# Kernel optimization log

Measured on AMD Instinct MI355X. Metric: run time of the kernel, lower is better.

The kernel has to match this reference:

```python
import jax, jax.numpy as jnp
import numpy as np

B, L, V, D, C, R = 8, 2048, 32000, 512, 64, 64
NBLK = 2           # n_layers - 1
H = 2 * D          # stem hidden dim
STD = 0.02


def _ln(x, w, b):
    m = x.mean(-1, keepdims=True)
    v = ((x - m) ** 2).mean(-1, keepdims=True)
    return (x - m) / jnp.sqrt(v + 1e-5) * w + b


def setup_inputs() -> dict:
    key = jax.random.key(0)
    ks = jax.random.split(key, 16)
    n = lambda k, shp: jax.random.normal(k, shp, dtype=jnp.float32) * STD
    return {
        "token_ids": jax.random.randint(ks[0], (B, L), 0, V),
        "tok_emb": n(ks[1], (V, D)),
        "pos_emb": n(ks[2], (L, D)),
        "stem_ln_w": jnp.ones((NBLK, D), jnp.float32),
        "stem_ln_b": jnp.zeros((NBLK, D), jnp.float32),
        "stem_w1": n(ks[3], (NBLK, D, H)),
        "stem_b1": jnp.zeros((NBLK, H), jnp.float32),
        "stem_w2": n(ks[4], (NBLK, H, D)),
        "stem_b2": jnp.zeros((NBLK, D), jnp.float32),
        "role_ln_w": jnp.ones((D,), jnp.float32),
        "role_ln_b": jnp.zeros((D,), jnp.float32),
        "Wa": n(ks[5], (D, R)),
        "Wb": n(ks[6], (D, R)),
        "Wc": n(ks[7], (D, R)),
        "class_a": n(ks[8], (C, R)),
        "class_b": n(ks[9], (C, R)),
        "class_c": n(ks[10], (C, R)),
        "query_ln_w": jnp.ones((D,), jnp.float32),
        "query_ln_b": jnp.zeros((D,), jnp.float32),
        "Wq": n(ks[11], (D, C)),
        "bq": jnp.zeros((C,), jnp.float32),
    }


def reference(token_ids, tok_emb, pos_emb, stem_ln_w, stem_ln_b, stem_w1,
              stem_b1, stem_w2, stem_b2, role_ln_w, role_ln_b, Wa, Wb, Wc,
              class_a, class_b, class_c, query_ln_w, query_ln_b, Wq, bq):
    seq_len = token_ids.shape[1]
    x = tok_emb[token_ids] + pos_emb[:seq_len][None, :, :]  # [B,L,D]
    for i in range(NBLK):
        h = _ln(x, stem_ln_w[i], stem_ln_b[i])
        h = jax.nn.gelu(h @ stem_w1[i] + stem_b1[i], approximate=False)
        x = x + h @ stem_w2[i] + stem_b2[i]
    prefix = _ln(x[:, :-1], role_ln_w, role_ln_b)  # [B,L-1,D]
    a = jnp.tanh(prefix @ Wa)
    b = jnp.tanh(prefix @ Wb)
    c = jnp.tanh(prefix @ Wc)
    ua = jnp.einsum('blr,cr->blc', a, class_a)  # [B,L-1,C]
    ub = jnp.einsum('blr,cr->blc', b, class_b)
    uc = jnp.einsum('blr,cr->blc', c, class_c)
    # exact ordered-triplet sum  sum_{i<j<k} ua_i * ub_j * uc_k  via exclusive cumsums
    prefA = jnp.cumsum(ua, axis=1) - ua            # sum_{i<j} ua_i
    t = ub * prefA
    prefT = jnp.cumsum(t, axis=1) - t              # sum_{j<k} ub_j * prefA_j
    s = (uc * prefT).sum(axis=1)                   # [B,C]
    Lp = max(seq_len - 1, 1)
    denom = max(Lp * (Lp - 1) * (Lp - 2) / 6.0, 1.0)
    q = _ln(x[:, -1], query_ln_w, query_ln_b)
    return s / denom + q @ Wq + bq
```

## Files before the change

### kernel.cpp

```cpp
#include <hip/hip_runtime.h>

#define NROWS 16384
#define LSEQ  2048
#define NB    8

typedef short v8s __attribute__((ext_vector_type(8)));
typedef float v4f __attribute__((ext_vector_type(4)));

__device__ __forceinline__ unsigned short f2bf(float f) {
    unsigned int u = __float_as_uint(f);
    return (unsigned short)((u + 0x7fffu + ((u >> 16) & 1u)) >> 16);
}
__device__ __forceinline__ float bf2f(unsigned short u) {
    return __uint_as_float(((unsigned int)u) << 16);
}

__device__ __forceinline__ void glds16(const void* g, void* l) {
    __builtin_amdgcn_global_load_lds(
        (__attribute__((address_space(1))) void*)g,
        (__attribute__((address_space(3))) void*)l,
        16, 0, 0);
}

__device__ __forceinline__ float fast_gelu(float v) {
    float z = fabsf(v) * 0.70710678118654752f;
    float t = __builtin_amdgcn_rcpf(1.0f + 0.3275911f * z);
    float poly = t * (0.254829592f + t * (-0.284496736f + t * (1.421413741f +
                 t * (-1.453152027f + t * 1.061405429f))));
    float erfz = 1.0f - poly * __expf(-z * z);
    float er = copysignf(erfz, v);
    return 0.5f * v * (1.0f + er);
}
__device__ __forceinline__ float fast_tanh(float y) {
    float e = __expf(2.0f * y);
    return (e - 1.0f) * __builtin_amdgcn_rcpf(e + 1.0f);
}

__device__ __forceinline__ long swizzled_row(int b, int wave) {
    int T = (b & 7) + (((b >> 3) & 15) << 3);
    int chunk = b >> 7;
    return (long)T * 128 + chunk * 4 + wave;
}

__global__ __launch_bounds__(256) void setup_kernel(
        const int* __restrict__ ids,
        const float* __restrict__ tok, const float* __restrict__ pos,
        const float* __restrict__ g0, const float* __restrict__ b0,
        const float* __restrict__ rolew, const float* __restrict__ roleb,
        const float* __restrict__ b1all,
        unsigned short* __restrict__ x, float* __restrict__ rowstat0,
        const float* __restrict__ w1, const float* __restrict__ w2,
        const float* __restrict__ wa, const float* __restrict__ wb, const float* __restrict__ wc,
        const float* __restrict__ ca, const float* __restrict__ cb, const float* __restrict__ cc,
        unsigned short* __restrict__ w1T, unsigned short* __restrict__ w2T,
        unsigned short* __restrict__ wabcT, unsigned short* __restrict__ clsb,
        float* __restrict__ c1buf, float* __restrict__ c2buf,
        float* __restrict__ c1a, float* __restrict__ c2a) {
    int blk = blockIdx.x;
    int t = threadIdx.x;
    if (blk < 4096) {
        int wave = t >> 6, lane = t & 63;
        long row = swizzled_row(blk, wave);
        int l = (int)(row & (LSEQ - 1));
        int id = ids[row];
        int d = lane * 8;
        float4 t0 = *(const float4*)(tok + (size_t)id * 512 + d);
        float4 t1 = *(const float4*)(tok + (size_t)id * 512 + d + 4);
        float4 p0 = *(const float4*)(pos + (size_t)l * 512 + d);
        float4 p1 = *(const float4*)(pos + (size_t)l * 512 + d + 4);
        float a[8] = {t0.x + p0.x, t0.y + p0.y, t0.z + p0.z, t0.w + p0.w,
                      t1.x + p1.x, t1.y + p1.y, t1.z + p1.z, t1.w + p1.w};
        unsigned int xp[4];
        #pragma unroll
        for (int i = 0; i < 4; ++i)
            xp[i] = (unsigned int)f2bf(a[2 * i]) | ((unsigned int)f2bf(a[2 * i + 1]) << 16);
        *(uint4*)(x + row * 512 + d) = *(uint4*)xp;
        float s = 0.f, s2 = 0.f;
        #pragma unroll
        for (int i = 0; i < 8; ++i) { s += a[i]; s2 += a[i] * a[i]; }
        #pragma unroll
        for (int o = 32; o > 0; o >>= 1) { s += __shfl_down(s, o); s2 += __shfl_down(s2, o); }
        if (lane == 0) {
            rowstat0[row * 2] = s;
            rowstat0[row * 2 + 1] = s2;
        }
    } else if (blk < 6240) {
        int id = blk - 4096;
        int tx = t & 31, ty = t >> 5;
        const float* in; unsigned short* out; int R, C, bx, by, ldo;
        const float* gfold = nullptr;
        if (id < 1024) {
            int l = id >> 9, r = id & 511;
            in = w1 + l * 524288; out = w1T + l * 524288;
            R = 512; C = 1024; bx = r & 31; by = r >> 5; ldo = 512;
            gfold = g0 + l * 512;
        } else if (id < 2048) {
            int l = (id - 1024) >> 9, r = (id - 1024) & 511;
            in = w2 + l * 524288; out = w2T + l * 524288;
            R = 1024; C = 512; bx = r & 15; by = r >> 4; ldo = 1024;
        } else {
            int g = (id - 2048) >> 5, r = (id - 2048) & 31;
            in = (g == 0) ? wa : (g == 1) ? wb : wc;
            out = wabcT + g * 32768;
            R = 512; C = 64; bx = r & 1; by = r >> 1; ldo = 512;
            gfold = rolew;
        }
        __shared__ unsigned short tile[32][33];
        int c0 = bx * 32, r0 = by * 32;
        for (int i = ty; i < 32; i += 8) {
            int r = r0 + i, c = c0 + tx;
            float v = (r < R && c < C) ? in[(size_t)r * C + c] : 0.f;
            if (gfold && r < R) v *= gfold[r];
            tile[i][tx] = f2bf(v);
        }
        __syncthreads();
        for (int i = ty; i < 32; i += 8) {
            int c = c0 + i, r = r0 + tx;
            if (r < R && c < C) out[(size_t)c * ldo + r] = tile[tx][i];
        }
    } else if (blk < 6243) {
        int g = blk - 6240;
        const float* src = (g == 0) ? ca : (g == 1) ? cb : cc;
        unsigned short* dst = clsb + g * 4096;
        for (int i = t; i < 4096; i += 256) dst[i] = f2bf(src[i]);
    } else if (blk < 6307) {
        int idx = blk - 6243;
        int l = idx >> 5, nch = idx & 31;
        int n = nch * 32 + (t & 31);
        int kq = t >> 5;
        const float* W = w1 + l * 524288;
        const float* g = g0 + l * 512;
        const float* b = b0 + l * 512;
        float a1 = 0.f, a2 = 0.f;
        for (int k = kq * 64; k < kq * 64 + 64; ++k) {
            float w = W[(size_t)k * 1024 + n];
            a1 += g[k] * w;
            a2 += b[k] * w;
        }
        __shared__ float red1[8][32], red2[8][32];
        red1[kq][t & 31] = a1;
        red2[kq][t & 31] = a2;
        __syncthreads();
        if (t < 32) {
            float s1 = 0.f, s2 = 0.f;
            #pragma unroll
            for (int q = 0; q < 8; ++q) { s1 += red1[q][t]; s2 += red2[q][t]; }
            int nn = nch * 32 + t;
            c1buf[l * 1024 + nn] = s1;
            c2buf[l * 1024 + nn] = s2 + b1all[l * 1024 + nn];
        }
    } else {
        int gi = blk - 6307;
        const float* W = (gi == 0) ? wa : (gi == 1) ? wb : wc;
        int n = t & 63, kq = t >> 6;
        float a1 = 0.f, a2 = 0.f;
        for (int k = kq * 128; k < kq * 128 + 128; ++k) {
            float w = W[(size_t)k * 64 + n];
            a1 += rolew[k] * w;
            a2 += roleb[k] * w;
        }
        __shared__ float red1[4][64], red2[4][64];
        red1[kq][n] = a1;
        red2[kq][n] = a2;
        __syncthreads();
        if (t < 64) {
            float s1 = 0.f, s2 = 0.f;
            #pragma unroll
            for (int q = 0; q < 4; ++q) { s1 += red1[q][t]; s2 += red2[q][t]; }
            c1a[gi * 64 + t] = s1;
            c2a[gi * 64 + t] = s2;
        }
    }
}

template <int SM>
__global__ __launch_bounds__(512, 1) void gemm_w1(
        const unsigned short* __restrict__ A,
        const unsigned short* __restrict__ BT,
        const float* __restrict__ c1, const float* __restrict__ c2,
        const float* __restrict__ stats,
        unsigned short* __restrict__ Cout) {
    constexpr int BN = 256, NFC = 4, FCH = 2, NLB = 2, BH = 128;
    constexpr int lda = 512, ldb = 512, ldc = 1024, K = 512;
    __shared__ unsigned short Ab[2][2][128 * 64] __attribute__((aligned(16)));
    __shared__ unsigned short Bb[2][2][BH * 64] __attribute__((aligned(16)));
    const int t = threadIdx.x;
    const int lane = t & 63, w = t >> 6;
    const int quad = lane >> 4, l16 = lane & 15;
    const int wmh = w >> 2;
    const int wn  = w & 3;
    const int bhalf = wn >> 1, bbase = (wn & 1) * (BN / 4);
    const long tileM = (long)blockIdx.x * 256;
    const long tileN = (long)blockIdx.y * BN;

    const int rl = lane >> 3;
    const int cl = ((lane & 7) ^ rl) * 8;

    const unsigned short* pa[2][2];
    #pragma unroll
    for (int h = 0; h < 2; ++h)
        #pragma unroll
        for (int q = 0; q < 2; ++q)
            pa[h][q] = A + (tileM + h * 128 + w * 16 + q * 8 + rl) * (size_t)lda + cl;
    const unsigned short* pb[2][2];
    #pragma unroll
    for (int h = 0; h < 2; ++h)
        #pragma unroll
        for (int q = 0; q < 2; ++q)
            pb[h][q] = BT + (tileN + h * BH + w * 16 + q * 8 + rl) * (size_t)ldb + cl;
    int kA = 0, kB = 0;

    auto stageA = [&](int buf, int h) {
        glds16(pa[h][0] + kA, &Ab[buf][h][(w * 2 + 0) * 512]);
        glds16(pa[h][1] + kA, &Ab[buf][h][(w * 2 + 1) * 512]);
    };
    auto stageB = [&](int buf, int h) {
        glds16(pb[h][0] + kB, &Bb[buf][h][(w * 2 + 0) * 512]);
        glds16(pb[h][1] + kB, &Bb[buf][h][(w * 2 + 1) * 512]);
    };

    const int xl = l16 & 7;
    const int ak0 = l16 * 64 + (((quad    ) ^ xl) * 8);
    const int ak1 = l16 * 64 + (((quad + 4) ^ xl) * 8);

    stageA(0, 0); stageA(0, 1); kA = 64;
    stageB(0, 0); stageB(0, 1); kB = 64;
    stageB(1, 0); stageB(1, 1); kB = 128;

    v4f acc[8][NFC] = {};
    const int nt = K >> 6;

    asm volatile("s_waitcnt vmcnt(%0)" :: "i"(2 * NLB) : "memory");
    __builtin_amdgcn_s_barrier();

    for (int tt = 0; tt < nt; ++tt) {
        const int bi = tt & 1;
        const unsigned short* Ah = &Ab[bi][wmh][0];
        const unsigned short* Bh = &Bb[bi][bhalf][bbase * 64];
        v8s af[4][2], bf[NFC][2];

        #pragma unroll
        for (int fr = 0; fr < 4; ++fr) {
            af[fr][0] = *(const v8s*)(Ah + fr * 1024 + ak0);
            af[fr][1] = *(const v8s*)(Ah + fr * 1024 + ak1);
        }
        #pragma unroll
        for (int fc = 0; fc < FCH; ++fc) {
            bf[fc][0] = *(const v8s*)(Bh + fc * 1024 + ak0);
            bf[fc][1] = *(const v8s*)(Bh + fc * 1024 + ak1);
        }
        if (tt + 1 < nt) stageA(bi ^ 1, 0);
        __builtin_amdgcn_s_barrier();
        asm volatile("s_waitcnt lgkmcnt(0)" ::: "memory");
        __builtin_amdgcn_s_setprio(1);
        #pragma unroll
        for (int fr = 0; fr < 4; ++fr)
            #pragma unroll
            for (int fc = 0; fc < FCH; ++fc) {
                acc[fr][fc] = __builtin_amdgcn_mfma_f32_16x16x32_bf16(bf[fc][0], af[fr][0], acc[fr][fc], 0, 0, 0);
                acc[fr][fc] = __builtin_amdgcn_mfma_f32_16x16x32_bf16(bf[fc][1], af[fr][1], acc[fr][fc], 0, 0, 0);
            }
        __builtin_amdgcn_s_setprio(0);
        __builtin_amdgcn_s_barrier();

        #pragma unroll
        for (int fc = FCH; fc < NFC; ++fc) {
            bf[fc][0] = *(const v8s*)(Bh + fc * 1024 + ak0);
            bf[fc][1] = *(const v8s*)(Bh + fc * 1024 + ak1);
        }
        if (tt + 1 < nt) stageA(bi ^ 1, 1);
        kA += 64;
        __builtin_amdgcn_s_barrier();
        asm volatile("s_waitcnt lgkmcnt(0)" ::: "memory");
        __builtin_amdgcn_s_setprio(1);
        #pragma unroll
        for (int fr = 0; fr < 4; ++fr)
            #pragma unroll
            for (int fc = FCH; fc < NFC; ++fc) {
                acc[fr][fc] = __builtin_amdgcn_mfma_f32_16x16x32_bf16(bf[fc][0], af[fr][0], acc[fr][fc], 0, 0, 0);
                acc[fr][fc] = __builtin_amdgcn_mfma_f32_16x16x32_bf16(bf[fc][1], af[fr][1], acc[fr][fc], 0, 0, 0);
            }
        __builtin_amdgcn_s_setprio(0);
        __builtin_amdgcn_s_barrier();

        #pragma unroll
        for (int fr = 0; fr < 4; ++fr) {
            af[fr][0] = *(const v8s*)(Ah + (fr + 4) * 1024 + ak0);
            af[fr][1] = *(const v8s*)(Ah + (fr + 4) * 1024 + ak1);
        }
        if (tt + 2 < nt) stageB(bi, 0);
        __builtin_amdgcn_s_barrier();
        asm volatile("s_waitcnt lgkmcnt(0)" ::: "memory");
        __builtin_amdgcn_s_setprio(1);
        #pragma unroll
        for (int fr = 0; fr < 4; ++fr)
            #pragma unroll
            for (int fc = 0; fc < FCH; ++fc) {
                acc[fr + 4][fc] = __builtin_amdgcn_mfma_f32_16x16x32_bf16(bf[fc][0], af[fr][0], acc[fr + 4][fc], 0, 0, 0);
                acc[fr + 4][fc] = __builtin_amdgcn_mfma_f32_16x16x32_bf16(bf[fc][1], af[fr][1], acc[fr + 4][fc], 0, 0, 0);
            }
        __builtin_amdgcn_s_setprio(0);
        __builtin_amdgcn_s_barrier();

        if (tt + 2 < nt) stageB(bi, 1);
        kB += 64;
        if (tt + 2 < nt)
            asm volatile("s_waitcnt vmcnt(%0)" :: "i"(2 * NLB) : "memory");
        else if (tt + 1 < nt)
            asm volatile("s_waitcnt vmcnt(0)" ::: "memory");
        __builtin_amdgcn_s_barrier();
        __builtin_amdgcn_s_setprio(1);
        #pragma unroll
        for (int fr = 0; fr < 4; ++fr)
            #pragma unroll
            for (int fc = FCH; fc < NFC; ++fc) {
                acc[fr + 4][fc] = __builtin_amdgcn_mfma_f32_16x16x32_bf16(bf[fc][0], af[fr][0], acc[fr + 4][fc], 0, 0, 0);
                acc[fr + 4][fc] = __builtin_amdgcn_mfma_f32_16x16x32_bf16(bf[fc][1], af[fr][1], acc[fr + 4][fc], 0, 0, 0);
            }
        __builtin_amdgcn_s_setprio(0);
        __builtin_amdgcn_s_barrier();
    }

    #pragma unroll
    for (int fr = 0; fr < 8; ++fr) {
        long m = tileM + wmh * 128 + fr * 16 + l16;
        float s1, s2;
        if (SM == 0) {
            float2 st = *(const float2*)&stats[m * 2];
            s1 = st.x; s2 = st.y;
        } else {
            float4 q0 = *(const float4*)&stats[m * 8];
            float4 q1 = *(const float4*)&stats[m * 8 + 4];
            s1 = q0.x + q0.z + q1.x + q1.z;
            s2 = q0.y + q0.w + q1.y + q1.w;
        }
        float mu = s1 * (1.0f / 512.0f);
        float rinv = 1.0f / sqrtf(s2 * (1.0f / 512.0f) - mu * mu + 1e-5f);
        float rmu = rinv * mu;
        #pragma unroll
        for (int fc = 0; fc < NFC; ++fc) {
            long n0 = tileN + wn * (BN / 4) + fc * 16 + quad * 4;
            float4 c14 = *(const float4*)&c1[n0];
            float4 c24 = *(const float4*)&c2[n0];
            const float* c1p = (const float*)&c14;
            const float* c2p = (const float*)&c24;
            unsigned short pk[4];
            #pragma unroll
            for (int r = 0; r < 4; ++r)
                pk[r] = f2bf(fast_gelu(rinv * acc[fr][fc][r] - rmu * c1p[r] + c2p[r]));
            *(ushort4*)&Cout[m * ldc + n0] = *(ushort4*)pk;
        }
    }
}

__global__ __launch_bounds__(512, 1) void gemm_w2(
        const unsigned short* __restrict__ A,
        const unsigned short* __restrict__ BT,
        const float* __restrict__ bias,
        unsigned short* __restrict__ x,
        float* __restrict__ rowpart) {
    constexpr int BN = 128, NFC = 2, FCH = 1, NLB = 1, BH = 64;
    constexpr int lda = 1024, ldb = 1024, K = 1024;
    __shared__ unsigned short Ab[2][2][128 * 64] __attribute__((aligned(16)));
    __shared__ unsigned short Bb[2][2][BH * 64] __attribute__((aligned(16)));
    const int t = threadIdx.x;
    const int lane = t & 63, w = t >> 6;
    const int quad = lane >> 4, l16 = lane & 15;
    const int wmh = w >> 2;
    const int wn  = w & 3;
    const int bhalf = wn >> 1, bbase = (wn & 1) * (BN / 4);
    const long tileM = (long)blockIdx.x * 256;
    const int yb = blockIdx.y;
    const long tileN = (long)yb * BN;

    const int rl = lane >> 3;
    const int cl = ((lane & 7) ^ rl) * 8;

    const unsigned short* pa[2][2];
    #pragma unroll
    for (int h = 0; h < 2; ++h)
        #pragma unroll
        for (int q = 0; q < 2; ++q)
            pa[h][q] = A + (tileM + h * 128 + w * 16 + q * 8 + rl) * (size_t)lda + cl;
    const unsigned short* pb[2];
    #pragma unroll
    for (int h = 0; h < 2; ++h)
        pb[h] = BT + (tileN + h * BH + w * 8 + rl) * (size_t)ldb + cl;
    int kA = 0, kB = 0;

    auto stageA = [&](int buf, int h) {
        glds16(pa[h][0] + kA, &Ab[buf][h][(w * 2 + 0) * 512]);
        glds16(pa[h][1] + kA, &Ab[buf][h][(w * 2 + 1) * 512]);
    };
    auto stageB = [&](int buf, int h) {
        glds16(pb[h] + kB, &Bb[buf][h][w * 512]);
    };

    const int xl = l16 & 7;
    const int ak0 = l16 * 64 + (((quad    ) ^ xl) * 8);
    const int ak1 = l16 * 64 + (((quad + 4) ^ xl) * 8);

    stageA(0, 0); stageA(0, 1); kA = 64;
    stageB(0, 0); stageB(0, 1); kB = 64;
    stageB(1, 0); stageB(1, 1); kB = 128;

    v4f acc[8][NFC] = {};
    const int nt = K >> 6;

    asm volatile("s_waitcnt vmcnt(%0)" :: "i"(2 * NLB) : "memory");
    __builtin_amdgcn_s_barrier();

    for (int tt = 0; tt < nt; ++tt) {
        const int bi = tt & 1;
        const unsigned short* Ah = &Ab[bi][wmh][0];
        const unsigned short* Bh = &Bb[bi][bhalf][bbase * 64];
        v8s af[4][2], bf[NFC][2];

        #pragma unroll
        for (int fr = 0; fr < 4; ++fr) {
            af[fr][0] = *(const v8s*)(Ah + fr * 1024 + ak0);
            af[fr][1] = *(const v8s*)(Ah + fr * 1024 + ak1);
        }
        #pragma unroll
        for (int fc = 0; fc < FCH; ++fc) {
            bf[fc][0] = *(const v8s*)(Bh + fc * 1024 + ak0);
            bf[fc][1] = *(const v8s*)(Bh + fc * 1024 + ak1);
        }
        if (tt + 1 < nt) stageA(bi ^ 1, 0);
        __builtin_amdgcn_s_barrier();
        asm volatile("s_waitcnt lgkmcnt(0)" ::: "memory");
        __builtin_amdgcn_s_setprio(1);
        #pragma unroll
        for (int fr = 0; fr < 4; ++fr)
            #pragma unroll
            for (int fc = 0; fc < FCH; ++fc) {
                acc[fr][fc] = __builtin_amdgcn_mfma_f32_16x16x32_bf16(bf[fc][0], af[fr][0], acc[fr][fc], 0, 0, 0);
                acc[fr][fc] = __builtin_amdgcn_mfma_f32_16x16x32_bf16(bf[fc][1], af[fr][1], acc[fr][fc], 0, 0, 0);
            }
        __builtin_amdgcn_s_setprio(0);
        __builtin_amdgcn_s_barrier();

        #pragma unroll
        for (int fc = FCH; fc < NFC; ++fc) {
            bf[fc][0] = *(const v8s*)(Bh + fc * 1024 + ak0);
            bf[fc][1] = *(const v8s*)(Bh + fc * 1024 + ak1);
        }
        if (tt + 1 < nt) stageA(bi ^ 1, 1);
        kA += 64;
        __builtin_amdgcn_s_barrier();
        asm volatile("s_waitcnt lgkmcnt(0)" ::: "memory");
        __builtin_amdgcn_s_setprio(1);
        #pragma unroll
        for (int fr = 0; fr < 4; ++fr)
            #pragma unroll
            for (int fc = FCH; fc < NFC; ++fc) {
                acc[fr][fc] = __builtin_amdgcn_mfma_f32_16x16x32_bf16(bf[fc][0], af[fr][0], acc[fr][fc], 0, 0, 0);
                acc[fr][fc] = __builtin_amdgcn_mfma_f32_16x16x32_bf16(bf[fc][1], af[fr][1], acc[fr][fc], 0, 0, 0);
            }
        __builtin_amdgcn_s_setprio(0);
        __builtin_amdgcn_s_barrier();

        #pragma unroll
        for (int fr = 0; fr < 4; ++fr) {
            af[fr][0] = *(const v8s*)(Ah + (fr + 4) * 1024 + ak0);
            af[fr][1] = *(const v8s*)(Ah + (fr + 4) * 1024 + ak1);
        }
        if (tt + 2 < nt) stageB(bi, 0);
        __builtin_amdgcn_s_barrier();
        asm volatile("s_waitcnt lgkmcnt(0)" ::: "memory");
        __builtin_amdgcn_s_setprio(1);
        #pragma unroll
        for (int fr = 0; fr < 4; ++fr)
            #pragma unroll
            for (int fc = 0; fc < FCH; ++fc) {
                acc[fr + 4][fc] = __builtin_amdgcn_mfma_f32_16x16x32_bf16(bf[fc][0], af[fr][0], acc[fr + 4][fc], 0, 0, 0);
                acc[fr + 4][fc] = __builtin_amdgcn_mfma_f32_16x16x32_bf16(bf[fc][1], af[fr][1], acc[fr + 4][fc], 0, 0, 0);
            }
        __builtin_amdgcn_s_setprio(0);
        __builtin_amdgcn_s_barrier();

        if (tt + 2 < nt) stageB(bi, 1);
        kB += 64;
        if (tt + 2 < nt)
            asm volatile("s_waitcnt vmcnt(%0)" :: "i"(2 * NLB) : "memory");
        else if (tt + 1 < nt)
            asm volatile("s_waitcnt vmcnt(0)" ::: "memory");
        __builtin_amdgcn_s_barrier();
        __builtin_amdgcn_s_setprio(1);
        #pragma unroll
        for (int fr = 0; fr < 4; ++fr)
            #pragma unroll
            for (int fc = FCH; fc < NFC; ++fc) {
                acc[fr + 4][fc] = __builtin_amdgcn_mfma_f32_16x16x32_bf16(bf[fc][0], af[fr][0], acc[fr + 4][fc], 0, 0, 0);
                acc[fr + 4][fc] = __builtin_amdgcn_mfma_f32_16x16x32_bf16(bf[fc][1], af[fr][1], acc[fr + 4][fc], 0, 0, 0);
            }
        __builtin_amdgcn_s_setprio(0);
        __builtin_amdgcn_s_barrier();
    }

    float p1[8], p2[8];
    #pragma unroll
    for (int fr = 0; fr < 8; ++fr) { p1[fr] = 0.f; p2[fr] = 0.f; }
    #pragma unroll
    for (int fr = 0; fr < 8; ++fr) {
        long m = tileM + wmh * 128 + fr * 16 + l16;
        #pragma unroll
        for (int fc = 0; fc < NFC; ++fc) {
            long n0 = tileN + wn * (BN / 4) + fc * 16 + quad * 4;
            float4 bi4 = *(const float4*)&bias[n0];
            const float* bip = (const float*)&bi4;
            ushort4 xr4 = *(const ushort4*)&x[m * 512 + n0];
            const unsigned short* xp = (const unsigned short*)&xr4;
            unsigned short pk[4];
            #pragma unroll
            for (int r = 0; r < 4; ++r) {
                float v = acc[fr][fc][r] + bip[r] + bf2f(xp[r]);
                p1[fr] += v; p2[fr] += v * v;
                pk[r] = f2bf(v);
            }
            *(ushort4*)&x[m * 512 + n0] = *(ushort4*)pk;
        }
    }
    #pragma unroll
    for (int fr = 0; fr < 8; ++fr) {
        p1[fr] += __shfl_xor(p1[fr], 16); p1[fr] += __shfl_xor(p1[fr], 32);
        p2[fr] += __shfl_xor(p2[fr], 16); p2[fr] += __shfl_xor(p2[fr], 32);
    }
    float* red = (float*)&Ab[0][0][0];
    if (quad == 0) {
        #pragma unroll
        for (int fr = 0; fr < 8; ++fr) {
            int r = wmh * 128 + fr * 16 + l16;
            red[r * 4 + wn] = p1[fr];
            red[1024 + r * 4 + wn] = p2[fr];
        }
    }
    __syncthreads();
    if (t < 256) {
        int r = t;
        float s1 = red[r * 4] + red[r * 4 + 1] + red[r * 4 + 2] + red[r * 4 + 3];
        float s2 = red[1024 + r * 4] + red[1024 + r * 4 + 1] + red[1024 + r * 4 + 2] + red[1024 + r * 4 + 3];
        long m = tileM + r;
        rowpart[m * 8 + yb * 2]     = s1;
        rowpart[m * 8 + yb * 2 + 1] = s2;
    }
}

__global__ __launch_bounds__(256) void tanh_scan_kernel(
        const unsigned short* __restrict__ A,
        const unsigned short* __restrict__ WT,
        const unsigned short* __restrict__ cls,
        const float* __restrict__ rowpart,
        const float* __restrict__ c1a, const float* __restrict__ c2a,
        float* __restrict__ part) {
    __shared__ unsigned short As[64][40] __attribute__((aligned(16)));
    __shared__ unsigned short Bs[3][64][40] __attribute__((aligned(16)));
    __shared__ unsigned short P[3][64 * 72] __attribute__((aligned(16)));
    __shared__ unsigned short U[64][200] __attribute__((aligned(16)));
    const int t = threadIdx.x;
    const int lane = t & 63, w = t >> 6;
    const int quad = lane >> 4, l16 = lane & 15;
    const long tileM = (long)blockIdx.x * 64;
    const int arow = t >> 2, acol = (t & 3) * 8;
    const int m = w * 16 + l16;

    const unsigned short* gA = A + (tileM + arow) * 512 + acol;
    const unsigned short* gB[3];
    #pragma unroll
    for (int g = 0; g < 3; ++g) gB[g] = WT + g * 32768 + arow * 512 + acol;

    v4f acc[3][4] = {};
    uint4 a0, b0[3];
    a0 = *(const uint4*)gA; gA += 32;
    #pragma unroll
    for (int g = 0; g < 3; ++g) { b0[g] = *(const uint4*)gB[g]; gB[g] += 32; }
    *(uint4*)&As[arow][acol] = a0;
    #pragma unroll
    for (int g = 0; g < 3; ++g) *(uint4*)&Bs[g][arow][acol] = b0[g];

    for (int kk = 0; kk < 16; ++kk) {
        __syncthreads();
        const bool more = kk < 15;
        if (more) {
            a0 = *(const uint4*)gA; gA += 32;
            #pragma unroll
            for (int g = 0; g < 3; ++g) { b0[g] = *(const uint4*)gB[g]; gB[g] += 32; }
        }
        v8s af = *(const v8s*)&As[m][quad * 8];
        #pragma unroll
        for (int g = 0; g < 3; ++g)
            #pragma unroll
            for (int fc = 0; fc < 4; ++fc) {
                v8s bfr = *(const v8s*)&Bs[g][fc * 16 + l16][quad * 8];
                acc[g][fc] = __builtin_amdgcn_mfma_f32_16x16x32_bf16(bfr, af, acc[g][fc], 0, 0, 0);
            }
        __syncthreads();
        if (more) {
            *(uint4*)&As[arow][acol] = a0;
            #pragma unroll
            for (int g = 0; g < 3; ++g) *(uint4*)&Bs[g][arow][acol] = b0[g];
        }
    }

    {
        long gm = tileM + m;
        float4 q0 = *(const float4*)&rowpart[gm * 8];
        float4 q1 = *(const float4*)&rowpart[gm * 8 + 4];
        float s1 = q0.x + q0.z + q1.x + q1.z;
        float s2 = q0.y + q0.w + q1.y + q1.w;
        float mu = s1 * (1.0f / 512.0f);
        float rinv = 1.0f / sqrtf(s2 * (1.0f / 512.0f) - mu * mu + 1e-5f);
        float rmu = rinv * mu;
        #pragma unroll
        for (int g = 0; g < 3; ++g)
            #pragma unroll
            for (int fc = 0; fc < 4; ++fc) {
                int n0 = fc * 16 + quad * 4;
                float4 c14 = *(const float4*)&c1a[g * 64 + n0];
                float4 c24 = *(const float4*)&c2a[g * 64 + n0];
                const float* c1p = (const float*)&c14;
                const float* c2p = (const float*)&c24;
                unsigned short pk[4];
                #pragma unroll
                for (int r = 0; r < 4; ++r)
                    pk[r] = f2bf(fast_tanh(rinv * acc[g][fc][r] - rmu * c1p[r] + c2p[r]));
                *(ushort4*)&P[g][m * 72 + n0] = *(ushort4*)pk;
            }
    }
    __syncthreads();

    #pragma unroll
    for (int g = 0; g < 3; ++g) {
        v4f acc2[4] = {};
        #pragma unroll
        for (int ks = 0; ks < 2; ++ks) {
            v8s paf = *(const v8s*)&P[g][m * 72 + ks * 32 + quad * 8];
            #pragma unroll
            for (int jc = 0; jc < 4; ++jc) {
                v8s cf = *(const v8s*)&cls[g * 4096 + (jc * 16 + l16) * 64 + ks * 32 + quad * 8];
                acc2[jc] = __builtin_amdgcn_mfma_f32_16x16x32_bf16(cf, paf, acc2[jc], 0, 0, 0);
            }
        }
        #pragma unroll
        for (int jc = 0; jc < 4; ++jc) {
            int c0 = jc * 16 + quad * 4;
            unsigned short pk[4];
            #pragma unroll
            for (int r = 0; r < 4; ++r) pk[r] = f2bf(acc2[jc][r]);
            *(ushort4*)&U[m][g * 64 + c0] = *(ushort4*)pk;
        }
    }
    __syncthreads();

    if (t < 64) {
        int c = t;
        int nl = (((int)(tileM & (LSEQ - 1))) == LSEQ - 64) ? 63 : 64;
        float sA = 0.f, sB = 0.f, sC = 0.f, T = 0.f, M = 0.f, Uu = 0.f;
        for (int l = 0; l < nl; ++l) {
            float ua = bf2f(U[l][c]);
            float ub = bf2f(U[l][64 + c]);
            float uc = bf2f(U[l][128 + c]);
            Uu += uc * T;
            M += uc * sB;
            T += ub * sA;
            sA += ua; sB += ub; sC += uc;
        }
        int b = (int)(tileM >> 11);
        int seg = (int)(tileM >> 6) & 31;
        float* p = part + ((size_t)(b * 32 + seg)) * 384 + c;
        p[0] = sA; p[64] = sB; p[128] = sC; p[192] = T; p[256] = M; p[320] = Uu;
    }
}

__global__ __launch_bounds__(64) void combine_final_kernel(const float* __restrict__ part,
        const unsigned short* __restrict__ x,
        const float* __restrict__ qw, const float* __restrict__ qb,
        const float* __restrict__ Wq, const float* __restrict__ bq,
        float* __restrict__ out, float inv_denom) {
    int b = blockIdx.x;
    int c = threadIdx.x;
    const float* p = part + (size_t)b * 32 * 384 + c;
    float A = p[0], B = p[64], Tt = p[192], Mt = p[256], Ut = p[320];
    for (int seg = 1; seg < 32; ++seg) {
        const float* q2 = p + seg * 384;
        float a2 = q2[0], b2 = q2[64], c2 = q2[128], t2 = q2[192], m2 = q2[256], u2 = q2[320];
        float Un = Ut + u2 + c2 * Tt + A * m2;
        float Tn = Tt + t2 + A * b2;
        float Mn = Mt + m2 + B * c2;
        A += a2; B += b2;
        Ut = Un; Tt = Tn; Mt = Mn;
    }
    __shared__ float q[512];
    __shared__ float mv[2];
    const unsigned short* xr = x + ((size_t)b * LSEQ + (LSEQ - 1)) * 512;
    float s1 = 0.f, s2 = 0.f;
    for (int i = c; i < 512; i += 64) { float v = bf2f(xr[i]); q[i] = v; s1 += v; s2 += v * v; }
    #pragma unroll
    for (int o = 32; o > 0; o >>= 1) { s1 += __shfl_down(s1, o); s2 += __shfl_down(s2, o); }
    if (c == 0) {
        float m = s1 * (1.0f / 512.0f);
        float var = s2 * (1.0f / 512.0f) - m * m;
        mv[0] = m; mv[1] = 1.0f / sqrtf(var + 1e-5f);
    }
    __syncthreads();
    float m = mv[0], r = mv[1];
    for (int i = c; i < 512; i += 64) q[i] = (q[i] - m) * r * qw[i] + qb[i];
    __syncthreads();
    float acc = 0.f;
    for (int d = 0; d < 512; ++d) acc += q[d] * Wq[d * 64 + c];
    out[b * 64 + c] = Ut * inv_denom + acc + bq[c];
}

extern "C" void kernel_launch(void* const* d_in, const int* in_sizes, int n_in,
                              void* d_out, int out_size, void* d_ws, size_t ws_size,
                              hipStream_t stream) {
    const int*   token_ids   = (const int*)d_in[0];
    const float* tok_emb     = (const float*)d_in[1];
    const float* pos_emb     = (const float*)d_in[2];
    const float* stem_ln_w   = (const float*)d_in[3];
    const float* stem_ln_b   = (const float*)d_in[4];
    const float* stem_w1     = (const float*)d_in[5];
    const float* stem_b1     = (const float*)d_in[6];
    const float* stem_w2     = (const float*)d_in[7];
    const float* stem_b2     = (const float*)d_in[8];
    const float* role_ln_w   = (const float*)d_in[9];
    const float* role_ln_b   = (const float*)d_in[10];
    const float* Wa          = (const float*)d_in[11];
    const float* Wb          = (const float*)d_in[12];
    const float* Wc          = (const float*)d_in[13];
    const float* class_a     = (const float*)d_in[14];
    const float* class_b     = (const float*)d_in[15];
    const float* class_c     = (const float*)d_in[16];
    const float* query_ln_w  = (const float*)d_in[17];
    const float* query_ln_b  = (const float*)d_in[18];
    const float* Wq          = (const float*)d_in[19];
    const float* bq          = (const float*)d_in[20];
    float* out = (float*)d_out;

    char* wsb = (char*)d_ws;
    unsigned short* x    = (unsigned short*)(wsb);
    unsigned short* Hb   = (unsigned short*)(wsb + 16777216);
    float* part          = (float*)(wsb + 50331648);
    unsigned short* w1T  = (unsigned short*)(wsb + 51118080);
    unsigned short* w2T  = (unsigned short*)(wsb + 53215232);
    unsigned short* wabcT= (unsigned short*)(wsb + 55312384);
    unsigned short* clsb = (unsigned short*)(wsb + 55508992);
    float* rowstat0      = (float*)(wsb + 55533568);
    float* rowpart1      = (float*)(wsb + 55664640);
    float* rowpart2      = (float*)(wsb + 56188928);
    float* c1buf         = (float*)(wsb + 56713216);
    float* c2buf         = (float*)(wsb + 56721408);
    float* c1a           = (float*)(wsb + 56729600);
    float* c2a           = (float*)(wsb + 56730368);

    setup_kernel<<<6310, 256, 0, stream>>>(token_ids, tok_emb, pos_emb,
        stem_ln_w, stem_ln_b, role_ln_w, role_ln_b, stem_b1,
        x, rowstat0,
        stem_w1, stem_w2, Wa, Wb, Wc, class_a, class_b, class_c,
        w1T, w2T, wabcT, clsb, c1buf, c2buf, c1a, c2a);

    gemm_w1<0><<<dim3(64, 4), 512, 0, stream>>>(
        x, w1T, c1buf, c2buf, rowstat0, Hb);
    gemm_w2<<<dim3(64, 4), 512, 0, stream>>>(
        Hb, w2T, stem_b2, x, rowpart1);
    gemm_w1<1><<<dim3(64, 4), 512, 0, stream>>>(
        x, w1T + 524288, c1buf + 1024, c2buf + 1024, rowpart1, Hb);
    gemm_w2<<<dim3(64, 4), 512, 0, stream>>>(
        Hb, w2T + 524288, stem_b2 + 512, x, rowpart2);

    tanh_scan_kernel<<<256, 256, 0, stream>>>(x, wabcT, clsb,
                                              rowpart2, c1a, c2a, part);

    float inv_denom = (float)(6.0 / (2047.0 * 2046.0 * 2045.0));
    combine_final_kernel<<<NB, 64, 0, stream>>>(part, x, query_ln_w, query_ln_b,
                                                Wq, bq, out, inv_denom);
}
```

Measured before the change: 326.6 us.

## Batch embedding rows per wave, parallelize tile scan across waves, swizzle scan tiles

The embedding part of setup now has each wave handle 4 rows, issuing all gathers before compute. That cuts the block count from 4096 to 1024 and exposes more memory-level parallelism. In tanh_scan_kernel the serial 64-row triplet scan, previously done by one wave, is split across four waves of 16 rows each, then merged with the associative segment-combine formula. The tile-to-block mapping is also permuted, which changes which tiles run concurrently and their L2 locality. The costs are more register pressure in setup and an extra LDS buffer plus a barrier in the scan.

```diff
diff --git a/kernel.cpp b/kernel.cpp
--- a/kernel.cpp
+++ b/kernel.cpp
@@ -34,12 +34,6 @@
 __device__ __forceinline__ float fast_tanh(float y) {
     float e = __expf(2.0f * y);
     return (e - 1.0f) * __builtin_amdgcn_rcpf(e + 1.0f);
-}
-
-__device__ __forceinline__ long swizzled_row(int b, int wave) {
-    int T = (b & 7) + (((b >> 3) & 15) << 3);
-    int chunk = b >> 7;
-    return (long)T * 128 + chunk * 4 + wave;
 }
 
 __global__ __launch_bounds__(256) void setup_kernel(
@@ -58,34 +52,62 @@
         float* __restrict__ c1a, float* __restrict__ c2a) {
     int blk = blockIdx.x;
     int t = threadIdx.x;
-    if (blk < 4096) {
+    if (blk < 1024) {
         int wave = t >> 6, lane = t & 63;
-        long row = swizzled_row(blk, wave);
-        int l = (int)(row & (LSEQ - 1));
-        int id = ids[row];
         int d = lane * 8;
-        float4 t0 = *(const float4*)(tok + (size_t)id * 512 + d);
-        float4 t1 = *(const float4*)(tok + (size_t)id * 512 + d + 4);
-        float4 p0 = *(const float4*)(pos + (size_t)l * 512 + d);
-        float4 p1 = *(const float4*)(pos + (size_t)l * 512 + d + 4);
-        float a[8] = {t0.x + p0.x, t0.y + p0.y, t0.z + p0.z, t0.w + p0.w,
-                      t1.x + p1.x, t1.y + p1.y, t1.z + p1.z, t1.w + p1.w};
-        unsigned int xp[4];
-        #pragma unroll
-        for (int i = 0; i < 4; ++i)
-            xp[i] = (unsigned int)f2bf(a[2 * i]) | ((unsigned int)f2bf(a[2 * i + 1]) << 16);
-        *(uint4*)(x + row * 512 + d) = *(uint4*)xp;
-        float s = 0.f, s2 = 0.f;
-        #pragma unroll
-        for (int i = 0; i < 8; ++i) { s += a[i]; s2 += a[i] * a[i]; }
-        #pragma unroll
-        for (int o = 32; o > 0; o >>= 1) { s += __shfl_down(s, o); s2 += __shfl_down(s2, o); }
+        int U = (blk & 7) | (((blk >> 3) & 7) << 3);
+        int chunk = blk >> 6;
+        long rowb = (long)U * 256 + chunk * 16 + wave * 4;
+        int id[4], lp[4];
+        #pragma unroll
+        for (int j = 0; j < 4; ++j) {
+            id[j] = ids[rowb + j];
+            lp[j] = (int)((rowb + j) & (LSEQ - 1));
+        }
+        float4 tv[4][2], pv[4][2];
+        #pragma unroll
+        for (int j = 0; j < 4; ++j) {
+            tv[j][0] = *(const float4*)(tok + (size_t)id[j] * 512 + d);
+            tv[j][1] = *(const float4*)(tok + (size_t)id[j] * 512 + d + 4);
+        }
+        #pragma unroll
+        for (int j = 0; j < 4; ++j) {
+            pv[j][0] = *(const float4*)(pos + (size_t)lp[j] * 512 + d);
+            pv[j][1] = *(const float4*)(pos + (size_t)lp[j] * 512 + d + 4);
+        }
+        float s1v[4], s2v[4];
+        #pragma unroll
+        for (int j = 0; j < 4; ++j) {
+            float a[8] = {tv[j][0].x + pv[j][0].x, tv[j][0].y + pv[j][0].y,
+                          tv[j][0].z + pv[j][0].z, tv[j][0].w + pv[j][0].w,
+                          tv[j][1].x + pv[j][1].x, tv[j][1].y + pv[j][1].y,
+                          tv[j][1].z + pv[j][1].z, tv[j][1].w + pv[j][1].w};
+            unsigned int xp[4];
+            #pragma unroll
+            for (int i = 0; i < 4; ++i)
+                xp[i] = (unsigned int)f2bf(a[2 * i]) | ((unsigned int)f2bf(a[2 * i + 1]) << 16);
+            *(uint4*)(x + (rowb + j) * 512 + d) = *(uint4*)xp;
+            float s = 0.f, s2 = 0.f;
+            #pragma unroll
+            for (int i = 0; i < 8; ++i) { s += a[i]; s2 += a[i] * a[i]; }
+            s1v[j] = s; s2v[j] = s2;
+        }
+        #pragma unroll
+        for (int o = 32; o > 0; o >>= 1)
+            #pragma unroll
+            for (int j = 0; j < 4; ++j) {
+                s1v[j] += __shfl_down(s1v[j], o);
+                s2v[j] += __shfl_down(s2v[j], o);
+            }
         if (lane == 0) {
-            rowstat0[row * 2] = s;
-            rowstat0[row * 2 + 1] = s2;
-        }
-    } else if (blk < 6240) {
-        int id = blk - 4096;
+            #pragma unroll
+            for (int j = 0; j < 4; ++j) {
+                rowstat0[(rowb + j) * 2]     = s1v[j];
+                rowstat0[(rowb + j) * 2 + 1] = s2v[j];
+            }
+        }
+    } else if (blk < 3168) {
+        int id = blk - 1024;
         int tx = t & 31, ty = t >> 5;
         const float* in; unsigned short* out; int R, C, bx, by, ldo;
         const float* gfold = nullptr;
@@ -118,13 +140,13 @@
             int c = c0 + i, r = r0 + tx;
             if (r < R && c < C) out[(size_t)c * ldo + r] = tile[tx][i];
         }
-    } else if (blk < 6243) {
-        int g = blk - 6240;
+    } else if (blk < 3171) {
+        int g = blk - 3168;
         const float* src = (g == 0) ? ca : (g == 1) ? cb : cc;
         unsigned short* dst = clsb + g * 4096;
         for (int i = t; i < 4096; i += 256) dst[i] = f2bf(src[i]);
-    } else if (blk < 6307) {
-        int idx = blk - 6243;
+    } else if (blk < 3235) {
+        int idx = blk - 3171;
         int l = idx >> 5, nch = idx & 31;
         int n = nch * 32 + (t & 31);
         int kq = t >> 5;
@@ -150,7 +172,7 @@
             c2buf[l * 1024 + nn] = s2 + b1all[l * 1024 + nn];
         }
     } else {
-        int gi = blk - 6307;
+        int gi = blk - 3235;
         const float* W = (gi == 0) ? wa : (gi == 1) ? wb : wc;
         int n = t & 63, kq = t >> 6;
         float a1 = 0.f, a2 = 0.f;
@@ -557,10 +579,13 @@
     __shared__ unsigned short Bs[3][64][40] __attribute__((aligned(16)));
     __shared__ unsigned short P[3][64 * 72] __attribute__((aligned(16)));
     __shared__ unsigned short U[64][200] __attribute__((aligned(16)));
+    __shared__ float ps[4][6][64];
     const int t = threadIdx.x;
     const int lane = t & 63, w = t >> 6;
     const int quad = lane >> 4, l16 = lane & 15;
-    const long tileM = (long)blockIdx.x * 64;
+    const int bi = blockIdx.x;
+    const int T = ((bi & 7) << 2) | ((bi >> 3) & 3) | (bi & 0xE0);
+    const long tileM = (long)T * 64;
     const int arow = t >> 2, acol = (t & 3) * 8;
     const int m = w * 16 + l16;
 
@@ -652,23 +677,43 @@
     }
     __syncthreads();
 
+    {
+        int c = lane;
+        int r0 = w * 16;
+        bool cut = (((int)(tileM & (LSEQ - 1))) == LSEQ - 64) && (w == 3);
+        int nl = cut ? 15 : 16;
+        float sA = 0.f, sB = 0.f, sC = 0.f, Tt = 0.f, M = 0.f, Uu = 0.f;
+        for (int l = 0; l < nl; ++l) {
+            float ua = bf2f(U[r0 + l][c]);
+            float ub = bf2f(U[r0 + l][64 + c]);
+            float uc = bf2f(U[r0 + l][128 + c]);
+            Uu += uc * Tt;
+            M += uc * sB;
+            Tt += ub * sA;
+            sA += ua; sB += ub; sC += uc;
+        }
+        ps[w][0][c] = sA; ps[w][1][c] = sB; ps[w][2][c] = sC;
+        ps[w][3][c] = Tt; ps[w][4][c] = M;  ps[w][5][c] = Uu;
+    }
+    __syncthreads();
     if (t < 64) {
         int c = t;
-        int nl = (((int)(tileM & (LSEQ - 1))) == LSEQ - 64) ? 63 : 64;
-        float sA = 0.f, sB = 0.f, sC = 0.f, T = 0.f, M = 0.f, Uu = 0.f;
-        for (int l = 0; l < nl; ++l) {
-            float ua = bf2f(U[l][c]);
-            float ub = bf2f(U[l][64 + c]);
-            float uc = bf2f(U[l][128 + c]);
-            Uu += uc * T;
-            M += uc * sB;
-            T += ub * sA;
-            sA += ua; sB += ub; sC += uc;
+        float A2 = ps[0][0][c], B2 = ps[0][1][c], C2 = ps[0][2][c];
+        float Tt = ps[0][3][c], M = ps[0][4][c], Uu = ps[0][5][c];
+        #pragma unroll
+        for (int wseg = 1; wseg < 4; ++wseg) {
+            float a2 = ps[wseg][0][c], b2 = ps[wseg][1][c], c2 = ps[wseg][2][c];
+            float t2 = ps[wseg][3][c], m2 = ps[wseg][4][c], u2 = ps[wseg][5][c];
+            float Un = Uu + u2 + c2 * Tt + A2 * m2;
+            float Tn = Tt + t2 + A2 * b2;
+            float Mn = M + m2 + B2 * c2;
+            A2 += a2; B2 += b2; C2 += c2;
+            Uu = Un; Tt = Tn; M = Mn;
         }
         int b = (int)(tileM >> 11);
         int seg = (int)(tileM >> 6) & 31;
         float* p = part + ((size_t)(b * 32 + seg)) * 384 + c;
-        p[0] = sA; p[64] = sB; p[128] = sC; p[192] = T; p[256] = M; p[320] = Uu;
+        p[0] = A2; p[64] = B2; p[128] = C2; p[192] = Tt; p[256] = M; p[320] = Uu;
     }
 }
 
@@ -753,7 +798,7 @@
     float* c1a           = (float*)(wsb + 56729600);
     float* c2a           = (float*)(wsb + 56730368);
 
-    setup_kernel<<<6310, 256, 0, stream>>>(token_ids, tok_emb, pos_emb,
+    setup_kernel<<<3238, 256, 0, stream>>>(token_ids, tok_emb, pos_emb,
         stem_ln_w, stem_ln_b, role_ln_w, role_ln_b, stem_b1,
         x, rowstat0,
         stem_w1, stem_w2, Wa, Wb, Wc, class_a, class_b, class_c,
```

Result: slower. 429.4 us (+31.5%).
